# Kernel tuning notes

Measured on AMD Instinct MI355X. Metric: run time of the kernel, lower is better.

## Reference

```python
import jax, jax.numpy as jnp
import numpy as np

NEG_BIG = -9e15

def setup_inputs() -> dict:
    key = jax.random.key(0)
    k1, k2, k3, k4 = jax.random.split(key, 4)
    B, N, C, D = 8, 2048, 128, 128
    x = jax.random.normal(k1, (B, N, C), dtype=jnp.float32)
    adj = jax.random.randint(k2, (N, N), 0, 2, dtype=jnp.int32)
    W = jax.random.normal(k3, (D, C), dtype=jnp.float32) * (1.0 / np.sqrt(C))
    a = jax.random.normal(k4, (1, 2 * D), dtype=jnp.float32) * (1.0 / np.sqrt(2 * D))
    return {"x": x, "adj": adj, "W": W, "a": a}

def reference(x, adj, W, a):
    # Wh: [B,N,D]
    Wh = jnp.einsum('bnc,dc->bnd', x, W)
    D = Wh.shape[-1]
    a1, a2 = a[0, :D], a[0, D:]
    # e[b,i,j] = leakyrelu(a1.Wh_i + a2.Wh_j)  (algebraic split of cat([Wh_i,Wh_j]) @ a)
    f1 = Wh @ a1  # [B,N]
    f2 = Wh @ a2  # [B,N]
    e = jax.nn.leaky_relu(f1[:, :, None] + f2[:, None, :], negative_slope=0.2)  # [B,N,N]
    e = jnp.where(adj[None] > 0, e, NEG_BIG)
    attention = jax.nn.softmax(e, axis=-1)
    h_prime = jnp.einsum('bij,bjd->bid', attention, Wh)
    return jax.nn.elu(h_prime)
```

## Files before the change

### kernel.cpp

```cpp
#include <hip/hip_runtime.h>
#include <hip/hip_bf16.h>
#include <math.h>

#define BB 8
#define NN 2048
#define CC 128
#define DD 128

typedef __attribute__((ext_vector_type(8))) short short8;
typedef __attribute__((ext_vector_type(4))) float f32x4;

static __device__ __forceinline__ unsigned short f2bf(float f) {
    __hip_bfloat16 h = __float2bfloat16(f);
    return *reinterpret_cast<unsigned short*>(&h);
}
static __device__ __forceinline__ float bf2f(unsigned short u) {
    __hip_bfloat16 h = *reinterpret_cast<__hip_bfloat16*>(&u);
    return __bfloat162float(h);
}

#define PACKB 256
__global__ __launch_bounds__(256) void prep_wh_kernel(
    const int* __restrict__ adj, unsigned int* __restrict__ padj,
    const float* __restrict__ x, const float* __restrict__ W,
    const float* __restrict__ a,
    unsigned short* __restrict__ WhbT,
    float* __restrict__ f1, float* __restrict__ E2g, float* __restrict__ G2g)
{
    __shared__ unsigned short Whs[128 * 136];
    __shared__ unsigned short Wls[128 * 136];
    const int bx  = blockIdx.x;
    const int tid = threadIdx.x;

    if (bx < PACKB) {
        const int wid = bx * 256 + tid;
        #pragma unroll
        for (int rep = 0; rep < 2; ++rep) {
            const int word = wid + rep * 65536;
            const int4* src = (const int4*)adj + (size_t)word * 8;
            unsigned int m = 0;
            #pragma unroll
            for (int k = 0; k < 8; ++k) {
                int4 v = src[k];
                m |= (v.x > 0 ? 1u : 0u) << (k * 4);
                m |= (v.y > 0 ? 1u : 0u) << (k * 4 + 1);
                m |= (v.z > 0 ? 1u : 0u) << (k * 4 + 2);
                m |= (v.w > 0 ? 1u : 0u) << (k * 4 + 3);
            }
            padj[word] = m;
        }
        return;
    }

    const int g  = bx - PACKB;
    const int b  = g & 7;
    const int n0 = (g >> 3) * 64;

    #pragma unroll
    for (int k = 0; k < 16; ++k) {
        const int e   = tid + 256 * k;
        float4 wv = *(const float4*)&W[e * 4];
        const int row = e >> 5;
        const int col = (e & 31) * 4;
        ushort4 hv, lv;
        hv.x = f2bf(wv.x); lv.x = f2bf(wv.x - bf2f(hv.x));
        hv.y = f2bf(wv.y); lv.y = f2bf(wv.y - bf2f(hv.y));
        hv.z = f2bf(wv.z); lv.z = f2bf(wv.z - bf2f(hv.z));
        hv.w = f2bf(wv.w); lv.w = f2bf(wv.w - bf2f(hv.w));
        *(ushort4*)&Whs[row * 136 + col] = hv;
        *(ushort4*)&Wls[row * 136 + col] = lv;
    }
    __syncthreads();

    const int w    = tid >> 6;
    const int lane = tid & 63;
    const int fr   = lane & 15, fk = lane >> 4;
    const int n    = n0 + w * 16 + fr;

    short8 bh[4], bl[4];
    const float* xrow = &x[((size_t)(b * NN) + n) * CC];
    #pragma unroll
    for (int ks = 0; ks < 4; ++ks) {
        float xv[8];
        *(float4*)&xv[0] = *(const float4*)&xrow[(ks * 4 + fk) * 8];
        *(float4*)&xv[4] = *(const float4*)&xrow[(ks * 4 + fk) * 8 + 4];
        #pragma unroll
        for (int e = 0; e < 8; ++e) {
            unsigned short h = f2bf(xv[e]);
            bh[ks][e] = (short)h;
            bl[ks][e] = (short)f2bf(xv[e] - bf2f(h));
        }
    }

    f32x4 acc[8];
    #pragma unroll
    for (int dt = 0; dt < 8; ++dt) acc[dt] = (f32x4){0.f, 0.f, 0.f, 0.f};

    #pragma unroll
    for (int dt = 0; dt < 8; ++dt) {
        #pragma unroll
        for (int ks = 0; ks < 4; ++ks) {
            const int off = (dt * 16 + fr) * 136 + (ks * 4 + fk) * 8;
            short8 aH = *(const short8*)&Whs[off];
            short8 aL = *(const short8*)&Wls[off];
            acc[dt] = __builtin_amdgcn_mfma_f32_16x16x32_bf16(aH, bh[ks], acc[dt], 0, 0, 0);
            acc[dt] = __builtin_amdgcn_mfma_f32_16x16x32_bf16(aH, bl[ks], acc[dt], 0, 0, 0);
            acc[dt] = __builtin_amdgcn_mfma_f32_16x16x32_bf16(aL, bh[ks], acc[dt], 0, 0, 0);
        }
    }

    float p1 = 0.f, p2 = 0.f;
    #pragma unroll
    for (int dt = 0; dt < 8; ++dt) {
        #pragma unroll
        for (int r = 0; r < 4; ++r) {
            const int d = dt * 16 + fk * 4 + r;
            p1 += acc[dt][r] * a[d];
            p2 += acc[dt][r] * a[DD + d];
        }
    }
    p1 += __shfl_xor(p1, 16); p1 += __shfl_xor(p1, 32);
    p2 += __shfl_xor(p2, 16); p2 += __shfl_xor(p2, 32);
    if (fk == 0) {
        f1[b * NN + n]  = p1;
        E2g[b * NN + n] = __expf(p2);
        G2g[b * NN + n] = __expf(0.2f * p2);
    }

    #pragma unroll
    for (int dt = 0; dt < 8; ++dt) {
        #pragma unroll
        for (int r = 0; r < 4; ++r) {
            const int d = dt * 16 + fk * 4 + r;
            WhbT[((size_t)(b * 128 + d)) * NN + n] = f2bf(acc[dt][r]);
        }
    }
}

template<int S, bool DIRECT>
__global__ __launch_bounds__(512) void gat_kernel(
    const unsigned short* __restrict__ WhbT,
    const unsigned int* __restrict__ padj,
    const float* __restrict__ f1,
    const float* __restrict__ E2g, const float* __restrict__ G2g,
    float* __restrict__ out,
    float* __restrict__ pPV, float* __restrict__ pS)
{
    constexpr int JS = NN / S;
    constexpr int NC = JS / 64;
    __shared__ __align__(16) unsigned short Bs[128 * 64];
    __shared__ __align__(16) unsigned short Ps[64 * 64];
    __shared__ float E2s[JS];
    __shared__ float G2s[JS];
    __shared__ float Srow[64];
    __shared__ float Sred[64];

    const int tid   = threadIdx.x;
    const int gblk  = blockIdx.x;
    const int b     = gblk & 7;
    const int rdec  = gblk >> 3;
    const int i0blk = rdec & 31;
    const int split = rdec >> 5;
    const int i0    = i0blk * 64;
    const int jBeg  = split * JS;

    #pragma unroll
    for (int k = 0; k < JS / 512; ++k) {
        E2s[tid + 512 * k] = E2g[b * NN + jBeg + tid + 512 * k];
        G2s[tid + 512 * k] = G2g[b * NN + jBeg + tid + 512 * k];
    }

    const int prow = tid >> 3;
    const int pjb  = tid & 7;
    const float f1r = f1[b * NN + i0 + prow];
    const float E1r = __expf(f1r);
    const float G1r = __expf(0.2f * f1r);
    const int psw = ((pjb ^ (prow & 7)) << 3);
    const unsigned int* padjRow = padj + (size_t)(i0 + prow) * 64 + (jBeg >> 5);

    const int w    = tid >> 6;
    const int wr   = w >> 2, wc = w & 3;
    const int lane = tid & 63;
    const int fr   = lane & 15;
    const int fk   = lane >> 4;
    f32x4 acc00 = {0.f,0.f,0.f,0.f}, acc01 = {0.f,0.f,0.f,0.f};
    f32x4 acc10 = {0.f,0.f,0.f,0.f}, acc11 = {0.f,0.f,0.f,0.f};
    float s_part = 0.f;

    const size_t wbase = (size_t)b * 128 * NN;
    const int g0 = tid,       gd0 = g0 >> 3, gj0 = (g0 & 7) * 8;
    const int g1 = tid + 512, gd1 = g1 >> 3, gj1 = (g1 & 7) * 8;
    const int sw0 = gd0 * 64 + ((((g0) & 7) ^ (gd0 & 7)) << 3);
    const int sw1 = gd1 * 64 + ((((g1) & 7) ^ (gd1 & 7)) << 3);

    uint4 br0 = *(const uint4*)&WhbT[wbase + (size_t)gd0 * NN + jBeg + gj0];
    uint4 br1 = *(const uint4*)&WhbT[wbase + (size_t)gd1 * NN + jBeg + gj1];
    unsigned int pw = padjRow[pjb >> 2];

    __syncthreads();

    for (int c = 0; c < NC; ++c) {
        float4 eA = *(const float4*)&E2s[c * 64 + pjb * 8];
        float4 eB = *(const float4*)&E2s[c * 64 + pjb * 8 + 4];
        float4 gA = *(const float4*)&G2s[c * 64 + pjb * 8];
        float4 gB = *(const float4*)&G2s[c * 64 + pjb * 8 + 4];
        float ev[8], gv[8];
        *(float4*)&ev[0] = eA; *(float4*)&ev[4] = eB;
        *(float4*)&gv[0] = gA; *(float4*)&gv[4] = gB;
        unsigned int pbits = (pw >> ((pjb & 3) << 3)) & 0xffu;
        unsigned short pks[8];
        float ssum = 0.f;
        #pragma unroll
        for (int e = 0; e < 8; ++e) {
            float m  = E1r * ev[e];
            float g  = G1r * gv[e];
            float wv = fmaxf(m, g);
            wv = ((pbits >> e) & 1u) ? wv : 0.f;
            unsigned short bw = f2bf(wv);
            pks[e] = bw;
            ssum += bf2f(bw);
        }
        s_part += ssum;

        if (c > 0) __syncthreads();
        *(uint4*)&Bs[sw0] = br0;
        *(uint4*)&Bs[sw1] = br1;
        {
            uint4 pv;
            pv.x = (unsigned int)pks[0] | ((unsigned int)pks[1] << 16);
            pv.y = (unsigned int)pks[2] | ((unsigned int)pks[3] << 16);
            pv.z = (unsigned int)pks[4] | ((unsigned int)pks[5] << 16);
            pv.w = (unsigned int)pks[6] | ((unsigned int)pks[7] << 16);
            *(uint4*)&Ps[prow * 64 + psw] = pv;
        }
        if (c + 1 < NC) {
            const int j0n = jBeg + (c + 1) * 64;
            br0 = *(const uint4*)&WhbT[wbase + (size_t)gd0 * NN + j0n + gj0];
            br1 = *(const uint4*)&WhbT[wbase + (size_t)gd1 * NN + j0n + gj1];
            pw  = padjRow[(c + 1) * 2 + (pjb >> 2)];
        }
        __syncthreads();
        __builtin_amdgcn_s_setprio(1);
        #pragma unroll
        for (int ks = 0; ks < 2; ++ks) {
            const int jbl = ks * 4 + fk;
            const int sb  = ((jbl ^ (fr & 7)) << 3);
            short8 aF0 = *(const short8*)&Ps[(wr * 32 + fr) * 64 + sb];
            short8 aF1 = *(const short8*)&Ps[(wr * 32 + 16 + fr) * 64 + sb];
            short8 bF0 = *(const short8*)&Bs[(wc * 32 + fr) * 64 + sb];
            short8 bF1 = *(const short8*)&Bs[(wc * 32 + 16 + fr) * 64 + sb];
            acc00 = __builtin_amdgcn_mfma_f32_16x16x32_bf16(aF0, bF0, acc00, 0, 0, 0);
            acc01 = __builtin_amdgcn_mfma_f32_16x16x32_bf16(aF0, bF1, acc01, 0, 0, 0);
            acc10 = __builtin_amdgcn_mfma_f32_16x16x32_bf16(aF1, bF0, acc10, 0, 0, 0);
            acc11 = __builtin_amdgcn_mfma_f32_16x16x32_bf16(aF1, bF1, acc11, 0, 0, 0);
        }
        __builtin_amdgcn_s_setprio(0);
    }

    {
        float v = s_part;
        v += __shfl_xor(v, 1); v += __shfl_xor(v, 2); v += __shfl_xor(v, 4);
        if (pjb == 0) Srow[prow] = v;
    }
    __syncthreads();
    if (tid < 64) {
        float st = Srow[tid];
        if (DIRECT) Sred[tid] = 1.0f / st;
        else        pS[(size_t)(b * S + split) * NN + i0 + tid] = st;
    }
    __syncthreads();

    if (DIRECT) {
        #pragma unroll
        for (int it = 0; it < 2; ++it) {
            #pragma unroll
            for (int dt = 0; dt < 2; ++dt) {
                f32x4 av = (it == 0) ? (dt == 0 ? acc00 : acc01)
                                     : (dt == 0 ? acc10 : acc11);
                #pragma unroll
                for (int r = 0; r < 4; ++r) {
                    int i = wr * 32 + it * 16 + fk * 4 + r;
                    int d = wc * 32 + dt * 16 + fr;
                    float hv = av[r] * Sred[i];
                    hv = (hv > 0.f) ? hv : expm1f(hv);
                    out[((size_t)(b * NN) + i0 + i) * DD + d] = hv;
                }
            }
        }
    } else {
        float* pbase = pPV + ((size_t)(b * S + split) * (NN / 64) + i0blk) * 8192;
        *(f32x4*)&pbase[(0 * 512 + tid) * 4] = acc00;
        *(f32x4*)&pbase[(1 * 512 + tid) * 4] = acc01;
        *(f32x4*)&pbase[(2 * 512 + tid) * 4] = acc10;
        *(f32x4*)&pbase[(3 * 512 + tid) * 4] = acc11;
    }
}

template<int S>
__global__ __launch_bounds__(512) void reduce_kernel(
    const float* __restrict__ pPV, const float* __restrict__ pS,
    float* __restrict__ out)
{
    __shared__ float T[64 * 132];
    __shared__ float Sred[64];

    const int tid   = threadIdx.x;
    const int gblk  = blockIdx.x;
    const int b     = gblk & 7;
    const int i0blk = gblk >> 3;
    const int i0    = i0blk * 64;

    if (tid < 64) {
        float st = 0.f;
        #pragma unroll
        for (int s = 0; s < S; ++s)
            st += pS[(size_t)(b * S + s) * NN + i0 + tid];
        Sred[tid] = 1.0f / st;
    }
    __syncthreads();

    const int w    = tid >> 6;
    const int wr   = w >> 2, wc = w & 3;
    const int lane = tid & 63;
    const int fr   = lane & 15, fk = lane >> 4;

    #pragma unroll
    for (int q = 0; q < 4; ++q) {
        f32x4 sum = {0.f, 0.f, 0.f, 0.f};
        #pragma unroll
        for (int s = 0; s < S; ++s) {
            const float* pbase = pPV +
                ((size_t)(b * S + s) * (NN / 64) + i0blk) * 8192;
            f32x4 v = *(const f32x4*)&pbase[(q * 512 + tid) * 4];
            sum[0] += v[0]; sum[1] += v[1]; sum[2] += v[2]; sum[3] += v[3];
        }
        const int it = q >> 1, dt = q & 1;
        #pragma unroll
        for (int r = 0; r < 4; ++r) {
            const int i = wr * 32 + it * 16 + fk * 4 + r;
            const int d = wc * 32 + dt * 16 + fr;
            float hv = sum[r] * Sred[i];
            hv = (hv > 0.f) ? hv : expm1f(hv);
            T[i * 132 + d] = hv;
        }
    }
    __syncthreads();

    #pragma unroll
    for (int k = 0; k < 4; ++k) {
        const int g   = tid + 512 * k;
        const int row = g >> 5;
        const int d4  = (g & 31) * 4;
        float4 h = *(const float4*)&T[row * 132 + d4];
        *(float4*)&out[((size_t)(b * NN) + i0 + row) * DD + d4] = h;
    }
}

extern "C" void kernel_launch(void* const* d_in, const int* in_sizes, int n_in,
                              void* d_out, int out_size, void* d_ws, size_t ws_size,
                              hipStream_t stream) {
    const float* x   = (const float*)d_in[0];
    const int*   adj = (const int*)d_in[1];
    const float* W   = (const float*)d_in[2];
    const float* a   = (const float*)d_in[3];
    float* out = (float*)d_out;

    char* p = (char*)d_ws;
    unsigned short* WhbT = (unsigned short*)p; p += (size_t)BB * NN * DD * 2;
    float* f1  = (float*)p; p += (size_t)BB * NN * 4;
    float* E2g = (float*)p; p += (size_t)BB * NN * 4;
    float* G2g = (float*)p; p += (size_t)BB * NN * 4;
    unsigned int* padj = (unsigned int*)p;    p += (size_t)NN * 64 * 4;
    float* pPV = (float*)p;

    const size_t base_bytes = (size_t)(p - (char*)d_ws);
    const size_t per_split  = (size_t)BB * NN * DD * 4 + (size_t)BB * NN * 4;

    prep_wh_kernel<<<PACKB + (NN / 64) * BB, 256, 0, stream>>>(
        adj, padj, x, W, a, WhbT, f1, E2g, G2g);

    if (ws_size >= base_bytes + 2 * per_split) {
        constexpr int S = 2;
        float* pS = pPV + (size_t)S * BB * NN * DD;
        gat_kernel<S, false><<<(NN / 64) * S * BB, 512, 0, stream>>>(
            WhbT, padj, f1, E2g, G2g, out, pPV, pS);
        reduce_kernel<S><<<(NN / 64) * BB, 512, 0, stream>>>(pPV, pS, out);
    } else {
        gat_kernel<1, true><<<(NN / 64) * BB, 512, 0, stream>>>(
            WhbT, padj, f1, E2g, G2g, out, nullptr, nullptr);
    }
}
```

Measured before the change: 39.09 us.

## Drop split-K reduce kernel; double-buffer LDS in single-pass GAT kernel

Removes the two-way j-split and its separate reduction kernel, so each block covers all 2048 columns and writes the normalized, ELU-applied output directly through an LDS transpose buffer, giving coalesced float4 stores. The main loop now ping-pongs two sets of B/P shared-memory buffers so the next chunk's probability computation and stores overlap the current chunk's MFMAs, leaving one barrier per chunk. This avoids writing and re-reading partial accumulators and saves a kernel launch. In exchange the grid shrinks to 256 blocks of 512 threads, which may underfill the GPU, and about 66KB of LDS per block limits occupancy.

```diff
diff --git a/kernel.cpp b/kernel.cpp
--- a/kernel.cpp
+++ b/kernel.cpp
@@ -137,37 +137,34 @@
     }
 }
 
-template<int S, bool DIRECT>
 __global__ __launch_bounds__(512) void gat_kernel(
     const unsigned short* __restrict__ WhbT,
     const unsigned int* __restrict__ padj,
     const float* __restrict__ f1,
     const float* __restrict__ E2g, const float* __restrict__ G2g,
-    float* __restrict__ out,
-    float* __restrict__ pPV, float* __restrict__ pS)
+    float* __restrict__ out)
 {
-    constexpr int JS = NN / S;
-    constexpr int NC = JS / 64;
-    __shared__ __align__(16) unsigned short Bs[128 * 64];
-    __shared__ __align__(16) unsigned short Ps[64 * 64];
-    __shared__ float E2s[JS];
-    __shared__ float G2s[JS];
-    __shared__ float Srow[64];
-    __shared__ float Sred[64];
-
-    const int tid   = threadIdx.x;
-    const int gblk  = blockIdx.x;
-    const int b     = gblk & 7;
-    const int rdec  = gblk >> 3;
-    const int i0blk = rdec & 31;
-    const int split = rdec >> 5;
-    const int i0    = i0blk * 64;
-    const int jBeg  = split * JS;
-
-    #pragma unroll
-    for (int k = 0; k < JS / 512; ++k) {
-        E2s[tid + 512 * k] = E2g[b * NN + jBeg + tid + 512 * k];
-        G2s[tid + 512 * k] = G2g[b * NN + jBeg + tid + 512 * k];
+    constexpr int NC = NN / 64;
+    __shared__ __align__(16) unsigned char smem[66048];
+    unsigned short* Bs0 = (unsigned short*)smem;
+    unsigned short* Bs1 = (unsigned short*)(smem + 16384);
+    unsigned short* Ps0 = (unsigned short*)(smem + 32768);
+    unsigned short* Ps1 = (unsigned short*)(smem + 40960);
+    float* E2s  = (float*)(smem + 49152);
+    float* G2s  = (float*)(smem + 57344);
+    float* Srow = (float*)(smem + 65536);
+    float* Sred = (float*)(smem + 65792);
+    float* T    = (float*)smem;
+
+    const int tid  = threadIdx.x;
+    const int gblk = blockIdx.x;
+    const int b    = gblk & 7;
+    const int i0   = (gblk >> 3) * 64;
+
+    #pragma unroll
+    for (int k = 0; k < NN / 512; ++k) {
+        E2s[tid + 512 * k] = E2g[b * NN + tid + 512 * k];
+        G2s[tid + 512 * k] = G2g[b * NN + tid + 512 * k];
     }
 
     const int prow = tid >> 3;
@@ -176,7 +173,7 @@
     const float E1r = __expf(f1r);
     const float G1r = __expf(0.2f * f1r);
     const int psw = ((pjb ^ (prow & 7)) << 3);
-    const unsigned int* padjRow = padj + (size_t)(i0 + prow) * 64 + (jBeg >> 5);
+    const unsigned int* padjRow = padj + (size_t)(i0 + prow) * 64;
 
     const int w    = tid >> 6;
     const int wr   = w >> 2, wc = w & 3;
@@ -193,69 +190,86 @@
     const int sw0 = gd0 * 64 + ((((g0) & 7) ^ (gd0 & 7)) << 3);
     const int sw1 = gd1 * 64 + ((((g1) & 7) ^ (gd1 & 7)) << 3);
 
-    uint4 br0 = *(const uint4*)&WhbT[wbase + (size_t)gd0 * NN + jBeg + gj0];
-    uint4 br1 = *(const uint4*)&WhbT[wbase + (size_t)gd1 * NN + jBeg + gj1];
-    unsigned int pw = padjRow[pjb >> 2];
-
-    __syncthreads();
-
-    for (int c = 0; c < NC; ++c) {
-        float4 eA = *(const float4*)&E2s[c * 64 + pjb * 8];
-        float4 eB = *(const float4*)&E2s[c * 64 + pjb * 8 + 4];
-        float4 gA = *(const float4*)&G2s[c * 64 + pjb * 8];
-        float4 gB = *(const float4*)&G2s[c * 64 + pjb * 8 + 4];
-        float ev[8], gv[8];
-        *(float4*)&ev[0] = eA; *(float4*)&ev[4] = eB;
-        *(float4*)&gv[0] = gA; *(float4*)&gv[4] = gB;
-        unsigned int pbits = (pw >> ((pjb & 3) << 3)) & 0xffu;
-        unsigned short pks[8];
-        float ssum = 0.f;
-        #pragma unroll
-        for (int e = 0; e < 8; ++e) {
-            float m  = E1r * ev[e];
-            float g  = G1r * gv[e];
-            float wv = fmaxf(m, g);
-            wv = ((pbits >> e) & 1u) ? wv : 0.f;
-            unsigned short bw = f2bf(wv);
-            pks[e] = bw;
-            ssum += bf2f(bw);
-        }
-        s_part += ssum;
-
-        if (c > 0) __syncthreads();
-        *(uint4*)&Bs[sw0] = br0;
-        *(uint4*)&Bs[sw1] = br1;
-        {
-            uint4 pv;
-            pv.x = (unsigned int)pks[0] | ((unsigned int)pks[1] << 16);
-            pv.y = (unsigned int)pks[2] | ((unsigned int)pks[3] << 16);
-            pv.z = (unsigned int)pks[4] | ((unsigned int)pks[5] << 16);
-            pv.w = (unsigned int)pks[6] | ((unsigned int)pks[7] << 16);
-            *(uint4*)&Ps[prow * 64 + psw] = pv;
-        }
-        if (c + 1 < NC) {
-            const int j0n = jBeg + (c + 1) * 64;
-            br0 = *(const uint4*)&WhbT[wbase + (size_t)gd0 * NN + j0n + gj0];
-            br1 = *(const uint4*)&WhbT[wbase + (size_t)gd1 * NN + j0n + gj1];
-            pw  = padjRow[(c + 1) * 2 + (pjb >> 2)];
-        }
+    uint4 brA0, brA1, brB0, brB1;
+    unsigned int pwA, pwB;
+
+#define LOADSET(s, c) do {                                                   \
+        br##s##0 = *(const uint4*)&WhbT[wbase + (size_t)gd0 * NN + (c) * 64 + gj0]; \
+        br##s##1 = *(const uint4*)&WhbT[wbase + (size_t)gd1 * NN + (c) * 64 + gj1]; \
+        pw##s    = padjRow[(c) * 2 + (pjb >> 2)];                            \
+    } while (0)
+
+#define PSTAGE(Bsb, Psb, s, c) do {                                          \
+        float4 eA = *(const float4*)&E2s[(c) * 64 + pjb * 8];                \
+        float4 eB = *(const float4*)&E2s[(c) * 64 + pjb * 8 + 4];            \
+        float4 gA = *(const float4*)&G2s[(c) * 64 + pjb * 8];                \
+        float4 gB = *(const float4*)&G2s[(c) * 64 + pjb * 8 + 4];            \
+        float ev[8], gv[8];                                                  \
+        *(float4*)&ev[0] = eA; *(float4*)&ev[4] = eB;                        \
+        *(float4*)&gv[0] = gA; *(float4*)&gv[4] = gB;                        \
+        unsigned int pbits = (pw##s >> ((pjb & 3) << 3)) & 0xffu;            \
+        unsigned short pks[8];                                               \
+        float ssum = 0.f;                                                    \
+        _Pragma("unroll")                                                    \
+        for (int e = 0; e < 8; ++e) {                                        \
+            float mv = E1r * ev[e];                                          \
+            float gg = G1r * gv[e];                                          \
+            float wv = fmaxf(mv, gg);                                        \
+            wv = ((pbits >> e) & 1u) ? wv : 0.f;                             \
+            unsigned short bw = f2bf(wv);                                    \
+            pks[e] = bw;                                                     \
+            ssum += bf2f(bw);                                                \
+        }                                                                    \
+        s_part += ssum;                                                      \
+        *(uint4*)&Bsb[sw0] = br##s##0;                                       \
+        *(uint4*)&Bsb[sw1] = br##s##1;                                       \
+        uint4 pv;                                                            \
+        pv.x = (unsigned int)pks[0] | ((unsigned int)pks[1] << 16);          \
+        pv.y = (unsigned int)pks[2] | ((unsigned int)pks[3] << 16);          \
+        pv.z = (unsigned int)pks[4] | ((unsigned int)pks[5] << 16);          \
+        pv.w = (unsigned int)pks[6] | ((unsigned int)pks[7] << 16);          \
+        *(uint4*)&Psb[prow * 64 + psw] = pv;                                 \
+    } while (0)
+
+#define MFMAC(Bsb, Psb) do {                                                 \
+        __builtin_amdgcn_s_setprio(1);                                       \
+        _Pragma("unroll")                                                    \
+        for (int ks = 0; ks < 2; ++ks) {                                     \
+            const int jbl = ks * 4 + fk;                                     \
+            const int sb  = ((jbl ^ (fr & 7)) << 3);                         \
+            short8 aF0 = *(const short8*)&Psb[(wr * 32 + fr) * 64 + sb];     \
+            short8 aF1 = *(const short8*)&Psb[(wr * 32 + 16 + fr) * 64 + sb];\
+            short8 bF0 = *(const short8*)&Bsb[(wc * 32 + fr) * 64 + sb];     \
+            short8 bF1 = *(const short8*)&Bsb[(wc * 32 + 16 + fr) * 64 + sb];\
+            acc00 = __builtin_amdgcn_mfma_f32_16x16x32_bf16(aF0, bF0, acc00, 0, 0, 0); \
+            acc01 = __builtin_amdgcn_mfma_f32_16x16x32_bf16(aF0, bF1, acc01, 0, 0, 0); \
+            acc10 = __builtin_amdgcn_mfma_f32_16x16x32_bf16(aF1, bF0, acc10, 0, 0, 0); \
+            acc11 = __builtin_amdgcn_mfma_f32_16x16x32_bf16(aF1, bF1, acc11, 0, 0, 0); \
+        }                                                                    \
+        __builtin_amdgcn_s_setprio(0);                                       \
+    } while (0)
+
+    LOADSET(A, 0);
+    __syncthreads();
+    PSTAGE(Bs0, Ps0, A, 0);
+    LOADSET(B, 1);
+    __syncthreads();
+
+    #pragma unroll 1
+    for (int cc = 0; cc < NC; cc += 2) {
+        PSTAGE(Bs1, Ps1, B, cc + 1);
+        if (cc + 2 < NC) LOADSET(A, cc + 2);
+        MFMAC(Bs0, Ps0);
         __syncthreads();
-        __builtin_amdgcn_s_setprio(1);
-        #pragma unroll
-        for (int ks = 0; ks < 2; ++ks) {
-            const int jbl = ks * 4 + fk;
-            const int sb  = ((jbl ^ (fr & 7)) << 3);
-            short8 aF0 = *(const short8*)&Ps[(wr * 32 + fr) * 64 + sb];
-            short8 aF1 = *(const short8*)&Ps[(wr * 32 + 16 + fr) * 64 + sb];
-            short8 bF0 = *(const short8*)&Bs[(wc * 32 + fr) * 64 + sb];
-            short8 bF1 = *(const short8*)&Bs[(wc * 32 + 16 + fr) * 64 + sb];
-            acc00 = __builtin_amdgcn_mfma_f32_16x16x32_bf16(aF0, bF0, acc00, 0, 0, 0);
-            acc01 = __builtin_amdgcn_mfma_f32_16x16x32_bf16(aF0, bF1, acc01, 0, 0, 0);
-            acc10 = __builtin_amdgcn_mfma_f32_16x16x32_bf16(aF1, bF0, acc10, 0, 0, 0);
-            acc11 = __builtin_amdgcn_mfma_f32_16x16x32_bf16(aF1, bF1, acc11, 0, 0, 0);
-        }
-        __builtin_amdgcn_s_setprio(0);
-    }
+        if (cc + 2 < NC) PSTAGE(Bs0, Ps0, A, cc + 2);
+        if (cc + 3 < NC) LOADSET(B, cc + 3);
+        MFMAC(Bs1, Ps1);
+        __syncthreads();
+    }
+
+#undef LOADSET
+#undef PSTAGE
+#undef MFMAC
 
     {
         float v = s_part;
@@ -263,85 +277,23 @@
         if (pjb == 0) Srow[prow] = v;
     }
     __syncthreads();
-    if (tid < 64) {
-        float st = Srow[tid];
-        if (DIRECT) Sred[tid] = 1.0f / st;
-        else        pS[(size_t)(b * S + split) * NN + i0 + tid] = st;
-    }
-    __syncthreads();
-
-    if (DIRECT) {
-        #pragma unroll
-        for (int it = 0; it < 2; ++it) {
+    if (tid < 64) Sred[tid] = 1.0f / Srow[tid];
+    __syncthreads();
+
+    #pragma unroll
+    for (int it = 0; it < 2; ++it) {
+        #pragma unroll
+        for (int dt = 0; dt < 2; ++dt) {
+            f32x4 av = (it == 0) ? (dt == 0 ? acc00 : acc01)
+                                 : (dt == 0 ? acc10 : acc11);
             #pragma unroll
-            for (int dt = 0; dt < 2; ++dt) {
-                f32x4 av = (it == 0) ? (dt == 0 ? acc00 : acc01)
-                                     : (dt == 0 ? acc10 : acc11);
-                #pragma unroll
-                for (int r = 0; r < 4; ++r) {
-                    int i = wr * 32 + it * 16 + fk * 4 + r;
-                    int d = wc * 32 + dt * 16 + fr;
-                    float hv = av[r] * Sred[i];
-                    hv = (hv > 0.f) ? hv : expm1f(hv);
-                    out[((size_t)(b * NN) + i0 + i) * DD + d] = hv;
-                }
+            for (int r = 0; r < 4; ++r) {
+                const int i = wr * 32 + it * 16 + fk * 4 + r;
+                const int d = wc * 32 + dt * 16 + fr;
+                float hv = av[r] * Sred[i];
+                hv = (hv > 0.f) ? hv : expm1f(hv);
+                T[i * 132 + d] = hv;
             }
-        }
-    } else {
-        float* pbase = pPV + ((size_t)(b * S + split) * (NN / 64) + i0blk) * 8192;
-        *(f32x4*)&pbase[(0 * 512 + tid) * 4] = acc00;
-        *(f32x4*)&pbase[(1 * 512 + tid) * 4] = acc01;
-        *(f32x4*)&pbase[(2 * 512 + tid) * 4] = acc10;
-        *(f32x4*)&pbase[(3 * 512 + tid) * 4] = acc11;
-    }
-}
-
-template<int S>
-__global__ __launch_bounds__(512) void reduce_kernel(
-    const float* __restrict__ pPV, const float* __restrict__ pS,
-    float* __restrict__ out)
-{
-    __shared__ float T[64 * 132];
-    __shared__ float Sred[64];
-
-    const int tid   = threadIdx.x;
-    const int gblk  = blockIdx.x;
-    const int b     = gblk & 7;
-    const int i0blk = gblk >> 3;
-    const int i0    = i0blk * 64;
-
-    if (tid < 64) {
-        float st = 0.f;
-        #pragma unroll
-        for (int s = 0; s < S; ++s)
-            st += pS[(size_t)(b * S + s) * NN + i0 + tid];
-        Sred[tid] = 1.0f / st;
-    }
-    __syncthreads();
-
-    const int w    = tid >> 6;
-    const int wr   = w >> 2, wc = w & 3;
-    const int lane = tid & 63;
-    const int fr   = lane & 15, fk = lane >> 4;
-
-    #pragma unroll
-    for (int q = 0; q < 4; ++q) {
-        f32x4 sum = {0.f, 0.f, 0.f, 0.f};
-        #pragma unroll
-        for (int s = 0; s < S; ++s) {
-            const float* pbase = pPV +
-                ((size_t)(b * S + s) * (NN / 64) + i0blk) * 8192;
-            f32x4 v = *(const f32x4*)&pbase[(q * 512 + tid) * 4];
-            sum[0] += v[0]; sum[1] += v[1]; sum[2] += v[2]; sum[3] += v[3];
-        }
-        const int it = q >> 1, dt = q & 1;
-        #pragma unroll
-        for (int r = 0; r < 4; ++r) {
-            const int i = wr * 32 + it * 16 + fk * 4 + r;
-            const int d = wc * 32 + dt * 16 + fr;
-            float hv = sum[r] * Sred[i];
-            hv = (hv > 0.f) ? hv : expm1f(hv);
-            T[i * 132 + d] = hv;
         }
     }
     __syncthreads();
@@ -371,22 +323,9 @@
     float* E2g = (float*)p; p += (size_t)BB * NN * 4;
     float* G2g = (float*)p; p += (size_t)BB * NN * 4;
     unsigned int* padj = (unsigned int*)p;    p += (size_t)NN * 64 * 4;
-    float* pPV = (float*)p;
-
-    const size_t base_bytes = (size_t)(p - (char*)d_ws);
-    const size_t per_split  = (size_t)BB * NN * DD * 4 + (size_t)BB * NN * 4;
 
     prep_wh_kernel<<<PACKB + (NN / 64) * BB, 256, 0, stream>>>(
         adj, padj, x, W, a, WhbT, f1, E2g, G2g);
-
-    if (ws_size >= base_bytes + 2 * per_split) {
-        constexpr int S = 2;
-        float* pS = pPV + (size_t)S * BB * NN * DD;
-        gat_kernel<S, false><<<(NN / 64) * S * BB, 512, 0, stream>>>(
-            WhbT, padj, f1, E2g, G2g, out, pPV, pS);
-        reduce_kernel<S><<<(NN / 64) * BB, 512, 0, stream>>>(pPV, pS, out);
-    } else {
-        gat_kernel<1, true><<<(NN / 64) * BB, 512, 0, stream>>>(
-            WhbT, padj, f1, E2g, G2g, out, nullptr, nullptr);
-    }
-}
+    gat_kernel<<<(NN / 64) * BB, 512, 0, stream>>>(
+        WhbT, padj, f1, E2g, G2g, out);
+}
```

New measurement: 37.02 us. -5.3%, faster.
